# Performance work log

Measured on AMD Instinct MI355X. Metric: run time of the kernel, lower is better.

Reference implementation:

```python
import jax, jax.numpy as jnp
import numpy as np

N_NODES = 100000
IN_CH, HID_CH, OUT_CH = 128, 128, 64
N_EDGES = 1600000


def gcn_conv(x, W, b, src, dst, num_nodes):
    """PyG GCNConv: x@W -> symmetric-normalized aggregation with self-loops -> +bias."""
    h = x @ W  # [N, out]
    loop = jnp.arange(num_nodes, dtype=src.dtype)
    src_a = jnp.concatenate([src, loop])  # add self-loops
    dst_a = jnp.concatenate([dst, loop])
    # degree of destination nodes over augmented edge set (edge_weight = 1)
    deg = jax.ops.segment_sum(jnp.ones_like(dst_a, dtype=h.dtype), dst_a,
                              num_segments=num_nodes)
    dis = jnp.where(deg > 0, jax.lax.rsqrt(jnp.maximum(deg, 1e-30)), 0.0)
    norm = dis[src_a] * dis[dst_a]  # [E+N]
    msg = h[src_a] * norm[:, None]  # gather + normalize
    out = jax.ops.segment_sum(msg, dst_a, num_segments=num_nodes)  # scatter-add
    return out + b


def setup_inputs() -> dict:
    key = jax.random.key(0)
    ks = jax.random.split(key, 9)
    x = jax.random.normal(ks[0], (N_NODES, IN_CH), dtype=jnp.float32)
    edge_index = jax.random.randint(ks[1], (2, N_EDGES), 0, N_NODES, dtype=jnp.int64)
    def glorot(k, fan_in, fan_out):
        s = np.sqrt(6.0 / (fan_in + fan_out)).astype(np.float32)
        return jax.random.uniform(k, (fan_in, fan_out), jnp.float32, -s, s)
    return {
        "x": x,
        "edge_index": edge_index,
        "W1": glorot(ks[2], IN_CH, HID_CH),
        "b1": jnp.zeros((HID_CH,), jnp.float32),
        "W2": glorot(ks[3], HID_CH, HID_CH),
        "b2": jnp.zeros((HID_CH,), jnp.float32),
        "Wo": glorot(ks[4], HID_CH, OUT_CH),
        "bo": jnp.zeros((OUT_CH,), jnp.float32),
    }


def reference(x, edge_index, W1, b1, W2, b2, Wo, bo):
    src, dst = edge_index[0], edge_index[1]
    n = x.shape[0]
    x1 = jax.nn.relu(gcn_conv(x, W1, b1, src, dst, n))
    x2 = jax.nn.relu(gcn_conv(x1, W2, b2, src, dst, n))
    return (x1 + x2) @ Wo + bo
```

## Files before the change

### kernel.cpp

```cpp
#include <hip/hip_runtime.h>
#include <hip/hip_fp16.h>

#define N_NODES 100000
#define N_EDGES 1600000
#define CH 128
#define OCH 64
#define NBUCKET 391
#define CAP 8192
#define BIN_CHUNK 4096

typedef _Float16 half8 __attribute__((ext_vector_type(8)));
typedef float f32x4 __attribute__((ext_vector_type(4)));

__device__ __forceinline__ ushort f2h(float f) {
    _Float16 h = (_Float16)f;
    return *(ushort*)&h;
}

__device__ __forceinline__ uint pkadd(uint a, uint b) {
    __half2 r = __hadd2(*(__half2*)&a, *(__half2*)&b);
    return *(uint*)&r;
}

__device__ __forceinline__ int swz(int row, int k) {
    return row * 128 + ((((k >> 3) ^ (row & 15)) << 3) | (k & 7));
}


__global__ __launch_bounds__(512) void k_bin(const int* __restrict__ src,
                                             const int* __restrict__ dst,
                                             int* __restrict__ bfill,
                                             int* __restrict__ bin) {
    __shared__ int hist[512];
    __shared__ int wbase[512];
    __shared__ int cur[512];
    const int t = threadIdx.x;
    const int e0 = blockIdx.x * BIN_CHUNK;

    hist[t] = 0;
    __syncthreads();

    int ss[8], bb[8], dl[8];
#pragma unroll
    for (int j = 0; j < 8; ++j) {
        int e = e0 + j * 512 + t;
        bb[j] = -1;
        if (e < N_EDGES) {
            int s = src[e], d = dst[e];
            ss[j] = s; dl[j] = d & 255; bb[j] = d >> 8;
            atomicAdd(&hist[bb[j]], 1);
        }
    }
    __syncthreads();

    int v = hist[t];
    for (int off = 1; off < 512; off <<= 1) {
        int tv = (t >= off) ? hist[t - off] : 0;
        __syncthreads();
        hist[t] += tv;
        __syncthreads();
    }
    int excl = hist[t] - v;
    if (t < NBUCKET && v > 0) {
        int gb = atomicAdd(&bfill[t], v);
        wbase[t] = gb - excl;
    }
    cur[t] = excl;
    __syncthreads();

#pragma unroll
    for (int j = 0; j < 8; ++j) {
        if (bb[j] >= 0) {
            int p = atomicAdd(&cur[bb[j]], 1);
            bin[bb[j] * CAP + wbase[bb[j]] + p] = (ss[j] << 8) | dl[j];
        }
    }
}

__global__ __launch_bounds__(512) void k_scan_prep(const int* __restrict__ bfill,
                                                   int* __restrict__ bbase,
                                                   const float* __restrict__ W1,
                                                   const float* __restrict__ W2,
                                                   const float* __restrict__ Wo,
                                                   ushort* __restrict__ W1s,
                                                   ushort* __restrict__ W2s,
                                                   ushort* __restrict__ WoTs) {
    if (blockIdx.x == 0) {
        __shared__ int tmp[512];
        int t = threadIdx.x;
        int v = (t < NBUCKET) ? bfill[t] : 0;
        tmp[t] = v;
        __syncthreads();
        for (int off = 1; off < 512; off <<= 1) {
            int tv = (t >= off) ? tmp[t - off] : 0;
            __syncthreads();
            tmp[t] += tv;
            __syncthreads();
        }
        if (t < NBUCKET) bbase[t] = tmp[t] - v;
    } else {
        int i = (blockIdx.x - 1) * 512 + threadIdx.x;
        if (i < 16384) {
            int k = i >> 7, n = i & 127;
            W1s[swz(n, k)] = f2h(W1[i]);
        } else if (i < 32768) {
            int j = i - 16384, k = j >> 7, n = j & 127;
            W2s[swz(n, k)] = f2h(W2[j]);
        } else if (i < 40960) {
            int j = i - 32768, k = j >> 6, n = j & 63;
            WoTs[swz(n, k)] = f2h(Wo[j]);
        }
    }
}

__global__ __launch_bounds__(256) void k_build(const int* __restrict__ bfill,
                                               const int* __restrict__ bbase,
                                               const int* __restrict__ bin,
                                               int* __restrict__ esrc,
                                               int* __restrict__ start,
                                               int* __restrict__ cnt,
                                               float* __restrict__ dis) {
    __shared__ int cnt_l[256];
    __shared__ int cur_l[256];
    __shared__ int sortbuf[CAP];
    const int t = threadIdx.x;
    const int b = blockIdx.x;
    const int n = bfill[b];
    const int base = bbase[b];
    const int* brec = bin + b * CAP;

    cnt_l[t] = 0;
    __syncthreads();
    for (int i = t; i < n; i += 256)
        atomicAdd(&cnt_l[brec[i] & 255], 1);
    __syncthreads();

    int v = cnt_l[t];
    for (int off = 1; off < 256; off <<= 1) {
        int tv = (t >= off) ? cnt_l[t - off] : 0;
        __syncthreads();
        cnt_l[t] += tv;
        __syncthreads();
    }
    int excl = cnt_l[t] - v;
    int node = b * 256 + t;
    if (node < N_NODES) {
        start[node] = base + excl;
        cnt[node] = v;
        dis[node] = rsqrtf((float)(v + 1));
    }
    cur_l[t] = excl;
    __syncthreads();

    for (int i = t; i < n; i += 256) {
        int rec = brec[i];
        int p = atomicAdd(&cur_l[rec & 255], 1);
        sortbuf[p] = rec >> 8;
    }
    __syncthreads();
    for (int i = t; i < n; i += 256)
        esrc[base + i] = sortbuf[i];
}


template <typename IT>
__global__ __launch_bounds__(256) void k_gemm_mfma(const IT* __restrict__ A,
                                                   const ushort* __restrict__ Ws,
                                                   const float* __restrict__ dis,
                                                   ushort* __restrict__ out) {
    __shared__ ushort sB[128 * 128];
    __shared__ ushort sA[64 * 128];
    const int tid = threadIdx.x;
    const int row0 = blockIdx.x * 64;

    for (int i = tid; i < 2048; i += 256)
        ((float4*)sB)[i] = ((const float4*)Ws)[i];

    for (int i = tid; i < 2048; i += 256) {
        int m = i >> 5, u = i & 31, k4 = u << 2;
        int r = row0 + m;
        ushort4 pk = make_ushort4(0, 0, 0, 0);
        if (r < N_NODES) {
            if constexpr (sizeof(IT) == 4) {
                float4 a = ((const float4*)A)[r * 32 + u];
                pk = make_ushort4(f2h(a.x), f2h(a.y), f2h(a.z), f2h(a.w));
            } else {
                pk = ((const ushort4*)A)[r * 32 + u];
            }
        }
        *(ushort4*)&sA[swz(m, k4)] = pk;
    }
    __syncthreads();

    const int lane = tid & 63, wv = tid >> 6;
    const int mrow = lane & 15, quad = lane >> 4;
    f32x4 acc[8] = {};
#pragma unroll
    for (int kc = 0; kc < 4; ++kc) {
        int g = kc * 4 + quad;
        half8 a = *(const half8*)&sA[(wv * 16 + mrow) * 128 + ((g ^ mrow) << 3)];
#pragma unroll
        for (int nt = 0; nt < 8; ++nt) {
            half8 b = *(const half8*)&sB[(nt * 16 + mrow) * 128 + ((g ^ mrow) << 3)];
            acc[nt] = __builtin_amdgcn_mfma_f32_16x16x32_f16(a, b, acc[nt], 0, 0, 0);
        }
    }

    const int rbase = row0 + wv * 16 + quad * 4;
    float ds[4];
#pragma unroll
    for (int rg = 0; rg < 4; ++rg)
        ds[rg] = (rbase + rg < N_NODES) ? dis[rbase + rg] : 0.f;
#pragma unroll
    for (int nt = 0; nt < 8; ++nt) {
#pragma unroll
        for (int rg = 0; rg < 4; ++rg) {
            int r = rbase + rg;
            if (r < N_NODES) out[r * 128 + nt * 16 + mrow] = f2h(acc[nt][rg] * ds[rg]);
        }
    }
}


__global__ __launch_bounds__(256) void k_agg(const int* __restrict__ start,
                                             const int* __restrict__ cnt,
                                             const int* __restrict__ esrc,
                                             const ushort* __restrict__ h,
                                             const float* __restrict__ dis,
                                             const float* __restrict__ bias,
                                             ushort* __restrict__ out) {
    const int v = blockIdx.x * 4 + (threadIdx.x >> 6);
    const int lane = threadIdx.x & 63, q = lane >> 4, l = lane & 15;
    const uint4* h16 = (const uint4*)h;

    int n = cnt[v];
    const int* ep = esrc + start[v];

    uint4 aA = make_uint4(0, 0, 0, 0), aB = make_uint4(0, 0, 0, 0);
    int i = q;
    for (; i + 12 < n; i += 16) {
        int s0 = ep[i], s1 = ep[i + 4], s2 = ep[i + 8], s3 = ep[i + 12];
        uint4 t0 = h16[s0 * 16 + l];
        uint4 t1 = h16[s1 * 16 + l];
        uint4 t2 = h16[s2 * 16 + l];
        uint4 t3 = h16[s3 * 16 + l];
        aA.x = pkadd(aA.x, t0.x); aA.y = pkadd(aA.y, t0.y);
        aA.z = pkadd(aA.z, t0.z); aA.w = pkadd(aA.w, t0.w);
        aB.x = pkadd(aB.x, t1.x); aB.y = pkadd(aB.y, t1.y);
        aB.z = pkadd(aB.z, t1.z); aB.w = pkadd(aB.w, t1.w);
        aA.x = pkadd(aA.x, t2.x); aA.y = pkadd(aA.y, t2.y);
        aA.z = pkadd(aA.z, t2.z); aA.w = pkadd(aA.w, t2.w);
        aB.x = pkadd(aB.x, t3.x); aB.y = pkadd(aB.y, t3.y);
        aB.z = pkadd(aB.z, t3.z); aB.w = pkadd(aB.w, t3.w);
    }
    for (; i < n; i += 4) {
        int s0 = ep[i];
        uint4 t0 = h16[s0 * 16 + l];
        aA.x = pkadd(aA.x, t0.x); aA.y = pkadd(aA.y, t0.y);
        aA.z = pkadd(aA.z, t0.z); aA.w = pkadd(aA.w, t0.w);
    }
    aA.x = pkadd(aA.x, aB.x); aA.y = pkadd(aA.y, aB.y);
    aA.z = pkadd(aA.z, aB.z); aA.w = pkadd(aA.w, aB.w);
    aA.x = pkadd(aA.x, (uint)__shfl_xor((int)aA.x, 16));
    aA.y = pkadd(aA.y, (uint)__shfl_xor((int)aA.y, 16));
    aA.z = pkadd(aA.z, (uint)__shfl_xor((int)aA.z, 16));
    aA.w = pkadd(aA.w, (uint)__shfl_xor((int)aA.w, 16));
    aA.x = pkadd(aA.x, (uint)__shfl_xor((int)aA.x, 32));
    aA.y = pkadd(aA.y, (uint)__shfl_xor((int)aA.y, 32));
    aA.z = pkadd(aA.z, (uint)__shfl_xor((int)aA.z, 32));
    aA.w = pkadd(aA.w, (uint)__shfl_xor((int)aA.w, 32));

    if (q == 0) {
        uint4 hv = h16[v * 16 + l];
        aA.x = pkadd(aA.x, hv.x); aA.y = pkadd(aA.y, hv.y);
        aA.z = pkadd(aA.z, hv.z); aA.w = pkadd(aA.w, hv.w);
        float s = dis[v];
        float2 a0 = __half22float2(*(__half2*)&aA.x);
        float2 a1 = __half22float2(*(__half2*)&aA.y);
        float2 a2 = __half22float2(*(__half2*)&aA.z);
        float2 a3 = __half22float2(*(__half2*)&aA.w);
        float4 b0 = ((const float4*)bias)[2 * l];
        float4 b1 = ((const float4*)bias)[2 * l + 1];
        a0.x = fmaxf(a0.x * s + b0.x, 0.f); a0.y = fmaxf(a0.y * s + b0.y, 0.f);
        a1.x = fmaxf(a1.x * s + b0.z, 0.f); a1.y = fmaxf(a1.y * s + b0.w, 0.f);
        a2.x = fmaxf(a2.x * s + b1.x, 0.f); a2.y = fmaxf(a2.y * s + b1.y, 0.f);
        a3.x = fmaxf(a3.x * s + b1.z, 0.f); a3.y = fmaxf(a3.y * s + b1.w, 0.f);
        __half2 o0 = __float22half2_rn(a0);
        __half2 o1 = __float22half2_rn(a1);
        __half2 o2 = __float22half2_rn(a2);
        __half2 o3 = __float22half2_rn(a3);
        ((uint4*)out)[v * 16 + l] =
            make_uint4(*(uint*)&o0, *(uint*)&o1, *(uint*)&o2, *(uint*)&o3);
    }
}


__global__ __launch_bounds__(256) void k_final_mfma(const ushort* __restrict__ x1,
                                                    const ushort* __restrict__ x2,
                                                    const ushort* __restrict__ Ws,
                                                    const float* __restrict__ bo,
                                                    float* __restrict__ out) {
    __shared__ ushort sB[64 * 128];
    __shared__ ushort sA[64 * 128];
    const int tid = threadIdx.x;
    const int row0 = blockIdx.x * 64;

    for (int i = tid; i < 1024; i += 256)
        ((float4*)sB)[i] = ((const float4*)Ws)[i];

    for (int i = tid; i < 2048; i += 256) {
        int m = i >> 5, u = i & 31, k4 = u << 2;
        int r = row0 + m;
        uint2 pk = make_uint2(0, 0);
        if (r < N_NODES) {
            uint2 ua = ((const uint2*)x1)[r * 32 + u];
            uint2 ub = ((const uint2*)x2)[r * 32 + u];
            __half2 s0 = __hadd2(*(__half2*)&ua.x, *(__half2*)&ub.x);
            __half2 s1 = __hadd2(*(__half2*)&ua.y, *(__half2*)&ub.y);
            pk = make_uint2(*(uint*)&s0, *(uint*)&s1);
        }
        *(uint2*)&sA[swz(m, k4)] = pk;
    }
    __syncthreads();

    const int lane = tid & 63, wv = tid >> 6;
    const int mrow = lane & 15, quad = lane >> 4;
    f32x4 acc[4] = {};
#pragma unroll
    for (int kc = 0; kc < 4; ++kc) {
        int g = kc * 4 + quad;
        half8 a = *(const half8*)&sA[(wv * 16 + mrow) * 128 + ((g ^ mrow) << 3)];
#pragma unroll
        for (int nt = 0; nt < 4; ++nt) {
            half8 b = *(const half8*)&sB[(nt * 16 + mrow) * 128 + ((g ^ mrow) << 3)];
            acc[nt] = __builtin_amdgcn_mfma_f32_16x16x32_f16(a, b, acc[nt], 0, 0, 0);
        }
    }

    const int rbase = row0 + wv * 16 + quad * 4;
#pragma unroll
    for (int nt = 0; nt < 4; ++nt) {
        float bb = bo[nt * 16 + mrow];
#pragma unroll
        for (int rg = 0; rg < 4; ++rg) {
            int r = rbase + rg;
            if (r < N_NODES) out[(size_t)r * 64 + nt * 16 + mrow] = acc[nt][rg] + bb;
        }
    }
}


extern "C" void kernel_launch(void* const* d_in, const int* in_sizes, int n_in,
                              void* d_out, int out_size, void* d_ws, size_t ws_size,
                              hipStream_t stream) {
    const float* x  = (const float*)d_in[0];
    const int*   ei = (const int*)d_in[1];
    const int*   src = ei;
    const int*   dst = ei + N_EDGES;
    const float* W1 = (const float*)d_in[2];
    const float* b1 = (const float*)d_in[3];
    const float* W2 = (const float*)d_in[4];
    const float* b2 = (const float*)d_in[5];
    const float* Wo = (const float*)d_in[6];
    const float* bo = (const float*)d_in[7];
    float* out = (float*)d_out;

    char* ws = (char*)d_ws;
    int*    bfill  = (int*)ws;            ws += 2048;
    int*    bbase  = (int*)ws;            ws += 2048;
    int*    cnt    = (int*)ws;            ws += 400000;
    int*    start  = (int*)ws;            ws += 400000;
    float*  dis    = (float*)ws;          ws += 400000;
    int*    bin    = (int*)ws;            ws += (size_t)NBUCKET * CAP * 4;
    int*    esrc   = (int*)ws;            ws += (size_t)N_EDGES * 4;
    ushort* W1s    = (ushort*)ws;         ws += 32768;
    ushort* W2s    = (ushort*)ws;         ws += 32768;
    ushort* WoTs   = (ushort*)ws;         ws += 16384;
    ushort* h      = (ushort*)ws;         ws += (size_t)N_NODES * CH * 2;
    ushort* x1     = (ushort*)ws;         ws += (size_t)N_NODES * CH * 2;
    ushort* x2     = (ushort*)ws;

    const int B = 256;
    const int gG = (N_NODES + 63) / 64;

    hipMemsetAsync(bfill, 0, 2048, stream);
    k_bin<<<(N_EDGES + BIN_CHUNK - 1) / BIN_CHUNK, 512, 0, stream>>>(src, dst, bfill, bin);
    k_scan_prep<<<81, 512, 0, stream>>>(bfill, bbase, W1, W2, Wo, W1s, W2s, WoTs);
    k_build<<<NBUCKET, 256, 0, stream>>>(bfill, bbase, bin, esrc, start, cnt, dis);

    k_gemm_mfma<float><<<gG, B, 0, stream>>>(x, W1s, dis, h);
    k_agg<<<N_NODES / 4, B, 0, stream>>>(start, cnt, esrc, h, dis, b1, x1);

    k_gemm_mfma<ushort><<<gG, B, 0, stream>>>(x1, W2s, dis, h);
    k_agg<<<N_NODES / 4, B, 0, stream>>>(start, cnt, esrc, h, dis, b2, x2);

    k_final_mfma<<<gG, B, 0, stream>>>(x1, x2, WoTs, bo, out);
}
```

Before: 334.8 us.

## Split hidden features into two column halves to shrink aggregation gather working set

The GEMM now writes h as two separate 64-column planes ([2][N][64] fp16), and the aggregation kernel runs twice as many blocks, each block gathering 8-byte chunks from a single half-plane. The goal is to halve the random-gather working set per pass so it fits the cache better, and to cut per-lane register use. Edge-index loads and output stores are marked nontemporal. The cost is that every edge list is read twice and each gather moves smaller 8-byte pieces.

```diff
diff --git a/kernel.cpp b/kernel.cpp
--- a/kernel.cpp
+++ b/kernel.cpp
@@ -8,9 +8,11 @@
 #define NBUCKET 391
 #define CAP 8192
 #define BIN_CHUNK 4096
+#define NBLK_AGG 25000
 
 typedef _Float16 half8 __attribute__((ext_vector_type(8)));
 typedef float f32x4 __attribute__((ext_vector_type(4)));
+typedef uint uint2v __attribute__((ext_vector_type(2)));
 
 __device__ __forceinline__ ushort f2h(float f) {
     _Float16 h = (_Float16)f;
@@ -213,10 +215,12 @@
         ds[rg] = (rbase + rg < N_NODES) ? dis[rbase + rg] : 0.f;
 #pragma unroll
     for (int nt = 0; nt < 8; ++nt) {
+        const size_t hbase = (size_t)(nt >> 2) * (N_NODES * 64);
+        const int c = (nt & 3) * 16 + mrow;
 #pragma unroll
         for (int rg = 0; rg < 4; ++rg) {
             int r = rbase + rg;
-            if (r < N_NODES) out[r * 128 + nt * 16 + mrow] = f2h(acc[nt][rg] * ds[rg]);
+            if (r < N_NODES) out[hbase + (size_t)r * 64 + c] = f2h(acc[nt][rg] * ds[rg]);
         }
     }
 }
@@ -229,68 +233,56 @@
                                              const float* __restrict__ dis,
                                              const float* __restrict__ bias,
                                              ushort* __restrict__ out) {
-    const int v = blockIdx.x * 4 + (threadIdx.x >> 6);
+    const int half = blockIdx.x / NBLK_AGG;
+    const int v = (blockIdx.x - half * NBLK_AGG) * 4 + (threadIdx.x >> 6);
     const int lane = threadIdx.x & 63, q = lane >> 4, l = lane & 15;
-    const uint4* h16 = (const uint4*)h;
+    const uint2v* h8 = (const uint2v*)(h + (size_t)half * (N_NODES * 64));
 
     int n = cnt[v];
     const int* ep = esrc + start[v];
 
-    uint4 aA = make_uint4(0, 0, 0, 0), aB = make_uint4(0, 0, 0, 0);
+    uint aAx = 0, aAy = 0, aBx = 0, aBy = 0;
     int i = q;
     for (; i + 12 < n; i += 16) {
-        int s0 = ep[i], s1 = ep[i + 4], s2 = ep[i + 8], s3 = ep[i + 12];
-        uint4 t0 = h16[s0 * 16 + l];
-        uint4 t1 = h16[s1 * 16 + l];
-        uint4 t2 = h16[s2 * 16 + l];
-        uint4 t3 = h16[s3 * 16 + l];
-        aA.x = pkadd(aA.x, t0.x); aA.y = pkadd(aA.y, t0.y);
-        aA.z = pkadd(aA.z, t0.z); aA.w = pkadd(aA.w, t0.w);
-        aB.x = pkadd(aB.x, t1.x); aB.y = pkadd(aB.y, t1.y);
-        aB.z = pkadd(aB.z, t1.z); aB.w = pkadd(aB.w, t1.w);
-        aA.x = pkadd(aA.x, t2.x); aA.y = pkadd(aA.y, t2.y);
-        aA.z = pkadd(aA.z, t2.z); aA.w = pkadd(aA.w, t2.w);
-        aB.x = pkadd(aB.x, t3.x); aB.y = pkadd(aB.y, t3.y);
-        aB.z = pkadd(aB.z, t3.z); aB.w = pkadd(aB.w, t3.w);
+        int s0 = __builtin_nontemporal_load(ep + i);
+        int s1 = __builtin_nontemporal_load(ep + i + 4);
+        int s2 = __builtin_nontemporal_load(ep + i + 8);
+        int s3 = __builtin_nontemporal_load(ep + i + 12);
+        uint2v t0 = h8[s0 * 16 + l];
+        uint2v t1 = h8[s1 * 16 + l];
+        uint2v t2 = h8[s2 * 16 + l];
+        uint2v t3 = h8[s3 * 16 + l];
+        aAx = pkadd(aAx, t0.x); aAy = pkadd(aAy, t0.y);
+        aBx = pkadd(aBx, t1.x); aBy = pkadd(aBy, t1.y);
+        aAx = pkadd(aAx, t2.x); aAy = pkadd(aAy, t2.y);
+        aBx = pkadd(aBx, t3.x); aBy = pkadd(aBy, t3.y);
     }
     for (; i < n; i += 4) {
-        int s0 = ep[i];
-        uint4 t0 = h16[s0 * 16 + l];
-        aA.x = pkadd(aA.x, t0.x); aA.y = pkadd(aA.y, t0.y);
-        aA.z = pkadd(aA.z, t0.z); aA.w = pkadd(aA.w, t0.w);
-    }
-    aA.x = pkadd(aA.x, aB.x); aA.y = pkadd(aA.y, aB.y);
-    aA.z = pkadd(aA.z, aB.z); aA.w = pkadd(aA.w, aB.w);
-    aA.x = pkadd(aA.x, (uint)__shfl_xor((int)aA.x, 16));
-    aA.y = pkadd(aA.y, (uint)__shfl_xor((int)aA.y, 16));
-    aA.z = pkadd(aA.z, (uint)__shfl_xor((int)aA.z, 16));
-    aA.w = pkadd(aA.w, (uint)__shfl_xor((int)aA.w, 16));
-    aA.x = pkadd(aA.x, (uint)__shfl_xor((int)aA.x, 32));
-    aA.y = pkadd(aA.y, (uint)__shfl_xor((int)aA.y, 32));
-    aA.z = pkadd(aA.z, (uint)__shfl_xor((int)aA.z, 32));
-    aA.w = pkadd(aA.w, (uint)__shfl_xor((int)aA.w, 32));
+        int s0 = __builtin_nontemporal_load(ep + i);
+        uint2v t0 = h8[s0 * 16 + l];
+        aAx = pkadd(aAx, t0.x); aAy = pkadd(aAy, t0.y);
+    }
+    aAx = pkadd(aAx, aBx); aAy = pkadd(aAy, aBy);
+    aAx = pkadd(aAx, (uint)__shfl_xor((int)aAx, 16));
+    aAy = pkadd(aAy, (uint)__shfl_xor((int)aAy, 16));
+    aAx = pkadd(aAx, (uint)__shfl_xor((int)aAx, 32));
+    aAy = pkadd(aAy, (uint)__shfl_xor((int)aAy, 32));
 
     if (q == 0) {
-        uint4 hv = h16[v * 16 + l];
-        aA.x = pkadd(aA.x, hv.x); aA.y = pkadd(aA.y, hv.y);
-        aA.z = pkadd(aA.z, hv.z); aA.w = pkadd(aA.w, hv.w);
+        uint2v hvv = h8[v * 16 + l];
+        uint hvx = hvv.x, hvy = hvv.y;
+        aAx = pkadd(aAx, hvx); aAy = pkadd(aAy, hvy);
         float s = dis[v];
-        float2 a0 = __half22float2(*(__half2*)&aA.x);
-        float2 a1 = __half22float2(*(__half2*)&aA.y);
-        float2 a2 = __half22float2(*(__half2*)&aA.z);
-        float2 a3 = __half22float2(*(__half2*)&aA.w);
-        float4 b0 = ((const float4*)bias)[2 * l];
-        float4 b1 = ((const float4*)bias)[2 * l + 1];
+        float2 a0 = __half22float2(*(__half2*)&aAx);
+        float2 a1 = __half22float2(*(__half2*)&aAy);
+        float4 b0 = ((const float4*)bias)[half * 16 + l];
         a0.x = fmaxf(a0.x * s + b0.x, 0.f); a0.y = fmaxf(a0.y * s + b0.y, 0.f);
         a1.x = fmaxf(a1.x * s + b0.z, 0.f); a1.y = fmaxf(a1.y * s + b0.w, 0.f);
-        a2.x = fmaxf(a2.x * s + b1.x, 0.f); a2.y = fmaxf(a2.y * s + b1.y, 0.f);
-        a3.x = fmaxf(a3.x * s + b1.z, 0.f); a3.y = fmaxf(a3.y * s + b1.w, 0.f);
         __half2 o0 = __float22half2_rn(a0);
         __half2 o1 = __float22half2_rn(a1);
-        __half2 o2 = __float22half2_rn(a2);
-        __half2 o3 = __float22half2_rn(a3);
-        ((uint4*)out)[v * 16 + l] =
-            make_uint4(*(uint*)&o0, *(uint*)&o1, *(uint*)&o2, *(uint*)&o3);
+        uint2v ov;
+        ov.x = *(uint*)&o0; ov.y = *(uint*)&o1;
+        __builtin_nontemporal_store(ov, (uint2v*)out + v * 32 + half * 16 + l);
     }
 }
 
@@ -389,10 +381,10 @@
     k_build<<<NBUCKET, 256, 0, stream>>>(bfill, bbase, bin, esrc, start, cnt, dis);
 
     k_gemm_mfma<float><<<gG, B, 0, stream>>>(x, W1s, dis, h);
-    k_agg<<<N_NODES / 4, B, 0, stream>>>(start, cnt, esrc, h, dis, b1, x1);
+    k_agg<<<2 * NBLK_AGG, B, 0, stream>>>(start, cnt, esrc, h, dis, b1, x1);
 
     k_gemm_mfma<ushort><<<gG, B, 0, stream>>>(x1, W2s, dis, h);
-    k_agg<<<N_NODES / 4, B, 0, stream>>>(start, cnt, esrc, h, dis, b2, x2);
+    k_agg<<<2 * NBLK_AGG, B, 0, stream>>>(start, cnt, esrc, h, dis, b2, x2);
 
     k_final_mfma<<<gG, B, 0, stream>>>(x1, x2, WoTs, bo, out);
 }
```

Result: slower. 442.5 us (+32.2%).

## Software-pipeline aggregation over four nodes per wave with zero-row padded gathers

Applied to the files above, without the earlier changes.

The aggregation kernel now has each wavefront handle four destination nodes. It overlaps the index loads and feature gathers of the next node with the accumulation of the previous one. The first 24 neighbours are gathered branch-free by pointing out-of-range slots at an extra zero row appended to h, and start/count are packed into one int2. This is meant to hide gather latency and cut per-node launch overhead, at the cost of more registers, lower occupancy, and extra wasted loads for low-degree nodes. The idx_stage reads of ep[q..q+20] can also go past the node's own range, though they stay within the esrc buffer.

```diff
diff --git a/kernel.cpp b/kernel.cpp
--- a/kernel.cpp
+++ b/kernel.cpp
@@ -8,6 +8,7 @@
 #define NBUCKET 391
 #define CAP 8192
 #define BIN_CHUNK 4096
+#define ZROW N_NODES
 
 typedef _Float16 half8 __attribute__((ext_vector_type(8)));
 typedef float f32x4 __attribute__((ext_vector_type(4)));
@@ -20,6 +21,12 @@
 __device__ __forceinline__ uint pkadd(uint a, uint b) {
     __half2 r = __hadd2(*(__half2*)&a, *(__half2*)&b);
     return *(uint*)&r;
+}
+
+__device__ __forceinline__ uint4 pk4(uint4 a, uint4 b) {
+    a.x = pkadd(a.x, b.x); a.y = pkadd(a.y, b.y);
+    a.z = pkadd(a.z, b.z); a.w = pkadd(a.w, b.w);
+    return a;
 }
 
 __device__ __forceinline__ int swz(int row, int k) {
@@ -117,8 +124,7 @@
                                                const int* __restrict__ bbase,
                                                const int* __restrict__ bin,
                                                int* __restrict__ esrc,
-                                               int* __restrict__ start,
-                                               int* __restrict__ cnt,
+                                               int2* __restrict__ scnt,
                                                float* __restrict__ dis) {
     __shared__ int cnt_l[256];
     __shared__ int cur_l[256];
@@ -145,8 +151,7 @@
     int excl = cnt_l[t] - v;
     int node = b * 256 + t;
     if (node < N_NODES) {
-        start[node] = base + excl;
-        cnt[node] = v;
+        scnt[node] = make_int2(base + excl, v);
         dis[node] = rsqrtf((float)(v + 1));
     }
     cur_l[t] = excl;
@@ -222,45 +227,64 @@
 }
 
 
-__global__ __launch_bounds__(256) void k_agg(const int* __restrict__ start,
-                                             const int* __restrict__ cnt,
-                                             const int* __restrict__ esrc,
-                                             const ushort* __restrict__ h,
-                                             const float* __restrict__ dis,
-                                             const float* __restrict__ bias,
-                                             ushort* __restrict__ out) {
-    const int v = blockIdx.x * 4 + (threadIdx.x >> 6);
-    const int lane = threadIdx.x & 63, q = lane >> 4, l = lane & 15;
-    const uint4* h16 = (const uint4*)h;
-
-    int n = cnt[v];
-    const int* ep = esrc + start[v];
-
+struct Ictx { int n; int grp; int s0, s1, s2, s3, s4, s5; };
+struct Gt { uint4 t0, t1, t2, t3, t4, t5, slf; };
+
+__device__ __forceinline__ Ictx idx_stage(const int* __restrict__ esrc, int off, int n, int q) {
+    Ictx c; c.n = n;
+    const int* ep = esrc + off;
+    int r0 = ep[q], r1 = ep[q + 4], r2 = ep[q + 8];
+    int r3 = ep[q + 12], r4 = ep[q + 16], r5 = ep[q + 20];
+    bool grp = (q + 12 < n);
+    bool ok = (n <= q + 24);
+    c.grp = grp;
+    c.s0 = (grp || q < n)      ? r0 : ZROW;
+    c.s1 = (grp || q + 4 < n)  ? r1 : ZROW;
+    c.s2 = (grp || q + 8 < n)  ? r2 : ZROW;
+    c.s3 = grp                 ? r3 : ZROW;
+    c.s4 = (grp && ok && q + 16 < n) ? r4 : ZROW;
+    c.s5 = (grp && ok && q + 20 < n) ? r5 : ZROW;
+    return c;
+}
+
+__device__ __forceinline__ Gt gather_stage(const Ictx& c, int v, int l,
+                                           const uint4* __restrict__ h16) {
+    Gt g;
+    g.t0 = h16[(size_t)c.s0 * 16 + l];
+    g.t1 = h16[(size_t)c.s1 * 16 + l];
+    g.t2 = h16[(size_t)c.s2 * 16 + l];
+    g.t3 = h16[(size_t)c.s3 * 16 + l];
+    g.t4 = h16[(size_t)c.s4 * 16 + l];
+    g.t5 = h16[(size_t)c.s5 * 16 + l];
+    g.slf = h16[(size_t)v * 16 + l];
+    return g;
+}
+
+__device__ __forceinline__ void acc_finish(const Gt& g, const Ictx& c, int v, int q, int l,
+                                           const int* __restrict__ esrc, int off,
+                                           const uint4* __restrict__ h16,
+                                           float dsv, float4 b0, float4 b1,
+                                           ushort* __restrict__ out) {
     uint4 aA = make_uint4(0, 0, 0, 0), aB = make_uint4(0, 0, 0, 0);
-    int i = q;
-    for (; i + 12 < n; i += 16) {
-        int s0 = ep[i], s1 = ep[i + 4], s2 = ep[i + 8], s3 = ep[i + 12];
-        uint4 t0 = h16[s0 * 16 + l];
-        uint4 t1 = h16[s1 * 16 + l];
-        uint4 t2 = h16[s2 * 16 + l];
-        uint4 t3 = h16[s3 * 16 + l];
-        aA.x = pkadd(aA.x, t0.x); aA.y = pkadd(aA.y, t0.y);
-        aA.z = pkadd(aA.z, t0.z); aA.w = pkadd(aA.w, t0.w);
-        aB.x = pkadd(aB.x, t1.x); aB.y = pkadd(aB.y, t1.y);
-        aB.z = pkadd(aB.z, t1.z); aB.w = pkadd(aB.w, t1.w);
-        aA.x = pkadd(aA.x, t2.x); aA.y = pkadd(aA.y, t2.y);
-        aA.z = pkadd(aA.z, t2.z); aA.w = pkadd(aA.w, t2.w);
-        aB.x = pkadd(aB.x, t3.x); aB.y = pkadd(aB.y, t3.y);
-        aB.z = pkadd(aB.z, t3.z); aB.w = pkadd(aB.w, t3.w);
-    }
-    for (; i < n; i += 4) {
-        int s0 = ep[i];
-        uint4 t0 = h16[s0 * 16 + l];
-        aA.x = pkadd(aA.x, t0.x); aA.y = pkadd(aA.y, t0.y);
-        aA.z = pkadd(aA.z, t0.z); aA.w = pkadd(aA.w, t0.w);
-    }
-    aA.x = pkadd(aA.x, aB.x); aA.y = pkadd(aA.y, aB.y);
-    aA.z = pkadd(aA.z, aB.z); aA.w = pkadd(aA.w, aB.w);
+    aA = pk4(aA, g.t0);
+    if (c.grp) aB = pk4(aB, g.t1); else aA = pk4(aA, g.t1);
+    aA = pk4(aA, g.t2);
+    if (c.grp) aB = pk4(aB, g.t3); else aA = pk4(aA, g.t3);
+    aA = pk4(aA, g.t4);
+    aA = pk4(aA, g.t5);
+    if (c.n > q + 24) {
+        const int* ep = esrc + off;
+        int i = q + 16;
+        for (; i + 12 < c.n; i += 16) {
+            uint4 u0 = h16[(size_t)ep[i] * 16 + l];
+            uint4 u1 = h16[(size_t)ep[i + 4] * 16 + l];
+            uint4 u2 = h16[(size_t)ep[i + 8] * 16 + l];
+            uint4 u3 = h16[(size_t)ep[i + 12] * 16 + l];
+            aA = pk4(aA, u0); aB = pk4(aB, u1); aA = pk4(aA, u2); aB = pk4(aB, u3);
+        }
+        for (; i < c.n; i += 4) aA = pk4(aA, h16[(size_t)ep[i] * 16 + l]);
+    }
+    aA = pk4(aA, aB);
     aA.x = pkadd(aA.x, (uint)__shfl_xor((int)aA.x, 16));
     aA.y = pkadd(aA.y, (uint)__shfl_xor((int)aA.y, 16));
     aA.z = pkadd(aA.z, (uint)__shfl_xor((int)aA.z, 16));
@@ -271,20 +295,15 @@
     aA.w = pkadd(aA.w, (uint)__shfl_xor((int)aA.w, 32));
 
     if (q == 0) {
-        uint4 hv = h16[v * 16 + l];
-        aA.x = pkadd(aA.x, hv.x); aA.y = pkadd(aA.y, hv.y);
-        aA.z = pkadd(aA.z, hv.z); aA.w = pkadd(aA.w, hv.w);
-        float s = dis[v];
+        aA = pk4(aA, g.slf);
         float2 a0 = __half22float2(*(__half2*)&aA.x);
         float2 a1 = __half22float2(*(__half2*)&aA.y);
         float2 a2 = __half22float2(*(__half2*)&aA.z);
         float2 a3 = __half22float2(*(__half2*)&aA.w);
-        float4 b0 = ((const float4*)bias)[2 * l];
-        float4 b1 = ((const float4*)bias)[2 * l + 1];
-        a0.x = fmaxf(a0.x * s + b0.x, 0.f); a0.y = fmaxf(a0.y * s + b0.y, 0.f);
-        a1.x = fmaxf(a1.x * s + b0.z, 0.f); a1.y = fmaxf(a1.y * s + b0.w, 0.f);
-        a2.x = fmaxf(a2.x * s + b1.x, 0.f); a2.y = fmaxf(a2.y * s + b1.y, 0.f);
-        a3.x = fmaxf(a3.x * s + b1.z, 0.f); a3.y = fmaxf(a3.y * s + b1.w, 0.f);
+        a0.x = fmaxf(a0.x * dsv + b0.x, 0.f); a0.y = fmaxf(a0.y * dsv + b0.y, 0.f);
+        a1.x = fmaxf(a1.x * dsv + b0.z, 0.f); a1.y = fmaxf(a1.y * dsv + b0.w, 0.f);
+        a2.x = fmaxf(a2.x * dsv + b1.x, 0.f); a2.y = fmaxf(a2.y * dsv + b1.y, 0.f);
+        a3.x = fmaxf(a3.x * dsv + b1.z, 0.f); a3.y = fmaxf(a3.y * dsv + b1.w, 0.f);
         __half2 o0 = __float22half2_rn(a0);
         __half2 o1 = __float22half2_rn(a1);
         __half2 o2 = __float22half2_rn(a2);
@@ -292,6 +311,36 @@
         ((uint4*)out)[v * 16 + l] =
             make_uint4(*(uint*)&o0, *(uint*)&o1, *(uint*)&o2, *(uint*)&o3);
     }
+}
+
+__global__ __launch_bounds__(256) void k_agg(const int2* __restrict__ scnt,
+                                             const int* __restrict__ esrc,
+                                             const ushort* __restrict__ h,
+                                             const float* __restrict__ dis,
+                                             const float* __restrict__ bias,
+                                             ushort* __restrict__ out) {
+    const int w = threadIdx.x >> 6;
+    const int vb = blockIdx.x * 16 + w * 4;
+    const int lane = threadIdx.x & 63, q = lane >> 4, l = lane & 15;
+    const uint4* h16 = (const uint4*)h;
+
+    int2 m0 = scnt[vb], m1 = scnt[vb + 1], m2 = scnt[vb + 2], m3 = scnt[vb + 3];
+    float d0 = dis[vb], d1 = dis[vb + 1], d2 = dis[vb + 2], d3 = dis[vb + 3];
+    float4 b0 = ((const float4*)bias)[2 * l];
+    float4 b1 = ((const float4*)bias)[2 * l + 1];
+
+    Ictx c0 = idx_stage(esrc, m0.x, m0.y, q);
+    Gt g0 = gather_stage(c0, vb, l, h16);
+    Ictx c1 = idx_stage(esrc, m1.x, m1.y, q);
+    Gt g1 = gather_stage(c1, vb + 1, l, h16);
+    Ictx c2 = idx_stage(esrc, m2.x, m2.y, q);
+    acc_finish(g0, c0, vb, q, l, esrc, m0.x, h16, d0, b0, b1, out);
+    Gt g2 = gather_stage(c2, vb + 2, l, h16);
+    Ictx c3 = idx_stage(esrc, m3.x, m3.y, q);
+    acc_finish(g1, c1, vb + 1, q, l, esrc, m1.x, h16, d1, b0, b1, out);
+    Gt g3 = gather_stage(c3, vb + 3, l, h16);
+    acc_finish(g2, c2, vb + 2, q, l, esrc, m2.x, h16, d2, b0, b1, out);
+    acc_finish(g3, c3, vb + 3, q, l, esrc, m3.x, h16, d3, b0, b1, out);
 }
 
 
@@ -368,31 +417,32 @@
     char* ws = (char*)d_ws;
     int*    bfill  = (int*)ws;            ws += 2048;
     int*    bbase  = (int*)ws;            ws += 2048;
-    int*    cnt    = (int*)ws;            ws += 400000;
-    int*    start  = (int*)ws;            ws += 400000;
+    int2*   scnt   = (int2*)ws;           ws += 800000;
     float*  dis    = (float*)ws;          ws += 400000;
     int*    bin    = (int*)ws;            ws += (size_t)NBUCKET * CAP * 4;
     int*    esrc   = (int*)ws;            ws += (size_t)N_EDGES * 4;
     ushort* W1s    = (ushort*)ws;         ws += 32768;
     ushort* W2s    = (ushort*)ws;         ws += 32768;
     ushort* WoTs   = (ushort*)ws;         ws += 16384;
-    ushort* h      = (ushort*)ws;         ws += (size_t)N_NODES * CH * 2;
+    ushort* h      = (ushort*)ws;         ws += (size_t)(N_NODES + 1) * CH * 2;
     ushort* x1     = (ushort*)ws;         ws += (size_t)N_NODES * CH * 2;
     ushort* x2     = (ushort*)ws;
 
     const int B = 256;
     const int gG = (N_NODES + 63) / 64;
+    const int gA = N_NODES / 16;
 
     hipMemsetAsync(bfill, 0, 2048, stream);
+    hipMemsetAsync(h + (size_t)N_NODES * CH, 0, CH * 2, stream);
     k_bin<<<(N_EDGES + BIN_CHUNK - 1) / BIN_CHUNK, 512, 0, stream>>>(src, dst, bfill, bin);
     k_scan_prep<<<81, 512, 0, stream>>>(bfill, bbase, W1, W2, Wo, W1s, W2s, WoTs);
-    k_build<<<NBUCKET, 256, 0, stream>>>(bfill, bbase, bin, esrc, start, cnt, dis);
+    k_build<<<NBUCKET, 256, 0, stream>>>(bfill, bbase, bin, esrc, scnt, dis);
 
     k_gemm_mfma<float><<<gG, B, 0, stream>>>(x, W1s, dis, h);
-    k_agg<<<N_NODES / 4, B, 0, stream>>>(start, cnt, esrc, h, dis, b1, x1);
+    k_agg<<<gA, B, 0, stream>>>(scnt, esrc, h, dis, b1, x1);
 
     k_gemm_mfma<ushort><<<gG, B, 0, stream>>>(x1, W2s, dis, h);
-    k_agg<<<N_NODES / 4, B, 0, stream>>>(start, cnt, esrc, h, dis, b2, x2);
+    k_agg<<<gA, B, 0, stream>>>(scnt, esrc, h, dis, b2, x2);
 
     k_final_mfma<<<gG, B, 0, stream>>>(x1, x2, WoTs, bo, out);
 }
```

New measurement: 337.0 us. No clear change (+0.7%).
